# Kernel tuning notes

Measured on AMD Instinct MI355X. Metric: run time of the kernel, lower is better.

Reference implementation:

```python
import jax, jax.numpy as jnp
import numpy as np
from jax import lax

HEADS = 8
HEAD_C = 16  # attention_channels // heads = 128 // 8


def setup_inputs() -> dict:
    key = jax.random.key(0)
    ks = jax.random.split(key, 16)
    N, I, H, W = 8, 128, 36, 36
    R, C, A, O = 128, 128, 128, 128  # recurrent, common, attention, out channels
    s = lambda *sh: 0.05
    inp = {
        'x': jax.random.normal(ks[0], (N, I, H, W), jnp.float32),
        # input 1x1 conv (Accumulate of single Conv, bias init 0)
        'w_in': jax.random.normal(ks[1], (R, I), jnp.float32) * 0.05,
        'b_in': jnp.zeros((R,), jnp.float32),
        # 3x3 conv on cat([x, h]) -> common channels
        'w_conv': jax.random.normal(ks[2], (C, 2 * R, 3, 3), jnp.float32) * 0.05,
        'b_conv': jnp.zeros((C,), jnp.float32),
        # q/k/v 1x1 projections (no bias)
        'wq': jax.random.normal(ks[3], (A, C), jnp.float32) * 0.05,
        'wk': jax.random.normal(ks[4], (A, C), jnp.float32) * 0.05,
        'wv': jax.random.normal(ks[5], (A, C), jnp.float32) * 0.05,
        # gate 1x1 projections on cat([z, a]) (C + A inputs)
        'w_i': jax.random.normal(ks[6], (R, C + A), jnp.float32) * 0.05,
        'b_i': jnp.full((R,), -1.0, jnp.float32),  # init_input
        'w_f': jax.random.normal(ks[7], (R, C + A), jnp.float32) * 0.05,
        'b_f': jnp.full((R,), 1.0, jnp.float32),   # init_forget
        'w_g': jax.random.normal(ks[8], (R, C + A), jnp.float32) * 0.05,
        'b_g': jnp.zeros((R,), jnp.float32),
        'w_o': jax.random.normal(ks[9], (R, C + A), jnp.float32) * 0.05,
        'b_o': jnp.zeros((R,), jnp.float32),
        # output 1x1 conv
        'w_out': jax.random.normal(ks[10], (O, R), jnp.float32) * 0.05,
        'b_out': jnp.zeros((O,), jnp.float32),
    }
    return inp


def _conv1x1(w, x, b=None):
    y = jnp.einsum('oi,nihw->nohw', w, x)
    if b is not None:
        y = y + b[None, :, None, None]
    return y


def reference(x, w_in, b_in, w_conv, b_conv, wq, wk, wv,
              w_i, b_i, w_f, b_f, w_g, b_g, w_o, b_o, w_out, b_out):
    # first timestep: past is empty -> h = c = 0
    xt = jnp.tanh(_conv1x1(w_in, x, b_in))          # [N, R, H, W]
    h0 = jnp.zeros_like(xt)
    c0 = jnp.zeros_like(xt)
    xh = jnp.concatenate([xt, h0], axis=1)          # groups=1 -> plain concat
    z = lax.conv_general_dilated(xh, w_conv, (1, 1), 'SAME') + b_conv[None, :, None, None]
    N, C, H, W = z.shape
    HW = H * W
    q = _conv1x1(wq, z).reshape(N, HEADS, HEAD_C, HW)
    k = _conv1x1(wk, z).reshape(N, HEADS, HEAD_C, HW)
    v = _conv1x1(wv, z).reshape(N, HEADS, HEAD_C, HW)
    # spatial attention over H*W tokens per head
    w_attn = jax.nn.softmax(jnp.einsum('nhcq,nhcd->nhqd', q, k), axis=-1)  # [N,heads,HW,HW]
    a = jnp.einsum('nhcd,nhqd->nhcq', v, w_attn).reshape(N, -1, H, W)      # [N,A,H,W]
    za = jnp.concatenate([z, a], axis=1)
    i = jax.nn.sigmoid(_conv1x1(w_i, za, b_i))
    f = jax.nn.sigmoid(_conv1x1(w_f, za, b_f))
    g = jnp.tanh(_conv1x1(w_g, za, b_g))
    o = jax.nn.sigmoid(_conv1x1(w_o, za, b_o))
    c = f * c0 + i * g
    h = o * jnp.tanh(c)  # dropout p=0 -> identity
    return _conv1x1(w_out, h, b_out)
```

## Files before the change

### kernel.cpp

```cpp
#include <hip/hip_runtime.h>
#include <hip/hip_bf16.h>
#include <math.h>

typedef __hip_bfloat16 bf16;
typedef __attribute__((ext_vector_type(8))) short frag8;
typedef __attribute__((ext_vector_type(4))) float f32x4;
typedef __attribute__((ext_vector_type(16))) float f32x16;
typedef __attribute__((ext_vector_type(2))) unsigned int u32x2;
typedef __attribute__((ext_vector_type(4))) unsigned int u32x4;

#define HW  1296
#define CH  128
#define TT  1327104

__device__ __forceinline__ float b2f(bf16 v) { return __bfloat162float(v); }
__device__ __forceinline__ float bits2f(unsigned short u) {
    return __uint_as_float(((unsigned)u) << 16);
}
__device__ __forceinline__ float frcp(float x) { return __builtin_amdgcn_rcpf(x); }
__device__ __forceinline__ float fsigm(float x) { return frcp(1.0f + __expf(-x)); }
__device__ __forceinline__ float ftanh(float x) {
    float xc = fminf(15.0f, fmaxf(-15.0f, x));
    float e = __expf(2.0f * xc);
    return (e - 1.0f) * frcp(e + 1.0f);
}
__device__ __forceinline__ int packrh(float a, float b) {
    unsigned ua = __float_as_uint(a) + 0x8000u;
    unsigned ub = __float_as_uint(b) + 0x8000u;
    return (int)__builtin_amdgcn_perm(ub, ua, 0x07060302);
}
__device__ __forceinline__ int2 pack4(float a, float b, float c, float d) {
    int2 r; r.x = packrh(a, b); r.y = packrh(c, d); return r;
}
__device__ __forceinline__ unsigned cvtpk(float a, float b) {
    unsigned r;
    asm("v_cvt_pk_bf16_f32 %0, %1, %2" : "=v"(r) : "v"(a), "v"(b));
    return r;
}

__device__ __forceinline__ int detect_f32(const void* w) {
    const short4* p = (const short4*)w;
    short4 v = p[threadIdx.x & 63];
    int bad = 0;
    #pragma unroll
    for (int j = 0; j < 4; ++j) {
        float f = bits2f(((const unsigned short*)&v)[j]);
        if (!(fabsf(f) <= 100.0f)) bad = 1;
    }
    return __any(bad) ? 1 : 0;
}

__global__ __launch_bounds__(256) void k_prep(
    const void* w_in, const void* w_conv, const void* wq, const void* wk, const void* wv,
    const void* w_i, const void* w_g, const void* w_o, const void* w_out,
    const void* b_in, const void* b_conv, const void* b_i, const void* b_g,
    const void* b_o, const void* b_out,
    bf16* __restrict__ Wdst, float* __restrict__ Bdst, bf16* __restrict__ Pad)
{
    int idx = blockIdx.x * 256 + threadIdx.x;
    const int f = detect_f32(w_in);
    if (idx < 327680) {
        const void* src; int si;
        if (idx < 16384)       { src = w_in; si = idx; }
        else if (idx < 163840) { int j = idx - 16384; int tap = j >> 14, rem = j & 16383;
                                 int o = rem >> 7, r = rem & 127;
                                 src = w_conv; si = o * 2304 + r * 9 + tap; }
        else if (idx < 212992) { int j = idx - 163840; int o = j >> 7, i = j & 127;
                                 int ws_ = o >> 7;
                                 src = ws_ == 0 ? wq : ws_ == 1 ? wk : wv;
                                 si = (o & 127) * 128 + i; }
        else if (idx < 311296) { int j = idx - 212992; int g = j >> 15, rem = j & 32767;
                                 int o = rem >> 8, k = rem & 255;
                                 src = g == 0 ? w_i : g == 1 ? w_g : w_o; si = o * 256 + k; }
        else                   { int j = idx - 311296; int o = j >> 7, i = j & 127;
                                 src = w_out; si = o * 128 + i; }
        float v = f ? ((const float*)src)[si] : b2f(((const bf16*)src)[si]);
        if (idx >= 163840 && idx < 180224) v *= 1.4426950408889634f;
        Wdst[idx] = __float2bfloat16(v);
    } else if (idx < 328448) {
        int j = idx - 327680; int b = j >> 7, e = j & 127;
        const void* src = b == 0 ? b_in : b == 1 ? b_conv : b == 2 ? b_i
                        : b == 3 ? b_g : b == 4 ? b_o : b_out;
        Bdst[j] = f ? ((const float*)src)[e] : b2f(((const bf16*)src)[e]);
    } else if (idx < 332544) {
        int j = idx - 328448;
        Pad[j] = __float2bfloat16(j < 2048 ? 0.0f : 1.0f);
    }
}

__global__ __launch_bounds__(256) void k_inm(const void* __restrict__ x,
                                             const void* __restrict__ wraw,
                                             const bf16* __restrict__ Wm,
                                             const float* __restrict__ bias,
                                             bf16* __restrict__ XT) {
    __shared__ short Xl[32][132];
    const int tid = threadIdx.x, wave = tid >> 6, lane = tid & 63;
    const int quad = lane >> 4, l16 = lane & 15;
    const int n = blockIdx.x;
    const int pbase = blockIdx.y * 32;
    const int obase = blockIdx.z * 32 + (wave & 1) * 16;
    const int pstrip = (wave >> 1) * 16;
    const int f = detect_f32(wraw);

    frag8 WF[4];
    #pragma unroll
    for (int kc = 0; kc < 4; ++kc)
        WF[kc] = *(const frag8*)&Wm[(obase + l16) * CH + kc * 32 + quad * 8];

    #pragma unroll
    for (int rep = 0; rep < 4; ++rep) {
        int u = tid + rep * 256;
        int i = u >> 3;
        int p4 = (u & 7) * 4;
        int p = pbase + p4;
        int pc = p < HW ? p : HW - 4;
        size_t gi = (size_t)n * CH * HW + (size_t)i * HW + pc;
        short4 s;
        if (f) {
            float4 fv = *(const float4*)((const float*)x + gi);
            int2 pk = pack4(fv.x, fv.y, fv.z, fv.w);
            s = *(short4*)&pk;
        } else {
            s = *(const short4*)((const bf16*)x + gi);
        }
        Xl[p4 + 0][i] = s.x; Xl[p4 + 1][i] = s.y;
        Xl[p4 + 2][i] = s.z; Xl[p4 + 3][i] = s.w;
    }
    __syncthreads();

    const int pl = pstrip + l16;
    f32x4 acc = {0.f, 0.f, 0.f, 0.f};
    #pragma unroll
    for (int kc = 0; kc < 4; ++kc) {
        int k = kc * 32 + quad * 8;
        short4 b0 = *(const short4*)&Xl[pl][k];
        short4 b1 = *(const short4*)&Xl[pl][k + 4];
        frag8 bf = {b0.x, b0.y, b0.z, b0.w, b1.x, b1.y, b1.z, b1.w};
        acc = __builtin_amdgcn_mfma_f32_16x16x32_bf16(WF[kc], bf, acc, 0, 0, 0);
    }

    int p = pbase + pstrip + l16;
    if (p < HW) {
        int og = obase + quad * 4;
        int2 pk = pack4(ftanh(acc[0] + bias[og + 0]), ftanh(acc[1] + bias[og + 1]),
                        ftanh(acc[2] + bias[og + 2]), ftanh(acc[3] + bias[og + 3]));
        *(int2*)((short*)XT + ((size_t)n * HW + p) * CH + og) = pk;
    }
}

__global__ __launch_bounds__(512) void k_cq(
    const bf16* __restrict__ XT, const bf16* __restrict__ Wc,
    const float* __restrict__ bc, const bf16* __restrict__ Wqkv,
    const bf16* __restrict__ Pad,
    bf16* __restrict__ Zb, bf16* __restrict__ Qb, bf16* __restrict__ Kb,
    bf16* __restrict__ Vb)
{
    __shared__ short Zl[32][136];
    __shared__ float Rd[4][4][4][64];
    const int tid = threadIdx.x, w = tid >> 6, lane = tid & 63;
    const int quad = lane >> 4, l16 = lane & 15;
    const int n = blockIdx.x;
    const int pbase = blockIdx.y * 32;
    const bf16* actn = XT + (size_t)n * HW * CH;

    const int o4 = w & 3, tg = w >> 2;
    const int obase = o4 * 32;
    const int p1 = pbase + l16, p2 = pbase + 16 + l16;
    const bool p1ok = p1 < HW, p2ok = p2 < HW;
    const int h1 = p1 / 36, w1 = p1 - h1 * 36;
    const int h2 = p2 / 36, w2 = p2 - h2 * 36;
    const bf16* zrow = Pad + quad * 8;

    f32x4 acc[2][2];
    #pragma unroll
    for (int of = 0; of < 2; ++of) {
        acc[of][0] = (f32x4){0.f, 0.f, 0.f, 0.f};
        acc[of][1] = (f32x4){0.f, 0.f, 0.f, 0.f};
    }

    const int tap0 = tg ? 5 : 0, tap1 = tg ? 9 : 5;
    for (int tap = tap0; tap < tap1; ++tap) {
        const int dy = tap / 3 - 1, dx = tap - (tap / 3) * 3 - 1;
        const bool ok1 = p1ok && (unsigned)(h1 + dy) < 36u && (unsigned)(w1 + dx) < 36u;
        const bool ok2 = p2ok && (unsigned)(h2 + dy) < 36u && (unsigned)(w2 + dx) < 36u;
        const int sh = dy * 36 + dx;
        const bf16* a1 = ok1 ? actn + (size_t)(p1 + sh) * CH + quad * 8 : zrow;
        const bf16* a2 = ok2 ? actn + (size_t)(p2 + sh) * CH + quad * 8 : zrow;
        const bf16* wp0 = Wc + tap * 16384 + (obase + l16) * CH + quad * 8;
        const bf16* wp1 = Wc + tap * 16384 + (obase + 16 + l16) * CH + quad * 8;
        frag8 A1[4], A2[4], W0[4], W1[4];
        #pragma unroll
        for (int kc = 0; kc < 4; ++kc) {
            A1[kc] = *(const frag8*)&a1[kc * 32];
            A2[kc] = *(const frag8*)&a2[kc * 32];
            W0[kc] = *(const frag8*)&wp0[kc * 32];
            W1[kc] = *(const frag8*)&wp1[kc * 32];
        }
        #pragma unroll
        for (int kc = 0; kc < 4; ++kc) {
            acc[0][0] = __builtin_amdgcn_mfma_f32_16x16x32_bf16(W0[kc], A1[kc], acc[0][0], 0, 0, 0);
            acc[0][1] = __builtin_amdgcn_mfma_f32_16x16x32_bf16(W0[kc], A2[kc], acc[0][1], 0, 0, 0);
            acc[1][0] = __builtin_amdgcn_mfma_f32_16x16x32_bf16(W1[kc], A1[kc], acc[1][0], 0, 0, 0);
            acc[1][1] = __builtin_amdgcn_mfma_f32_16x16x32_bf16(W1[kc], A2[kc], acc[1][1], 0, 0, 0);
        }
    }

    if (tg == 1) {
        #pragma unroll
        for (int of = 0; of < 2; ++of)
            #pragma unroll
            for (int pt = 0; pt < 2; ++pt)
                #pragma unroll
                for (int r = 0; r < 4; ++r)
                    Rd[o4][of * 2 + pt][r][lane] = acc[of][pt][r];
    }
    __syncthreads();
    if (tg == 0) {
        #pragma unroll
        for (int of = 0; of < 2; ++of) {
            #pragma unroll
            for (int pt = 0; pt < 2; ++pt) {
                #pragma unroll
                for (int r = 0; r < 4; ++r)
                    acc[of][pt][r] += Rd[o4][of * 2 + pt][r][lane];
                int og = obase + of * 16 + quad * 4;
                int pl = pt * 16 + l16;
                int p = pbase + pl;
                int2 pk = pack4(acc[of][pt][0] + bc[og + 0], acc[of][pt][1] + bc[og + 1],
                                acc[of][pt][2] + bc[og + 2], acc[of][pt][3] + bc[og + 3]);
                *(int2*)&Zl[pl][og] = pk;
                if (p < HW)
                    *(int2*)((short*)Zb + ((size_t)n * HW + p) * CH + og) = pk;
            }
        }
    }
    __syncthreads();

    for (int ot = w; ot < 12; ot += 8) {
        const bool vt = (ot >= 8);
        const int ob = ot * 32;
        frag8 B1[4], B2[4], W0a[4], W1a[4];
        #pragma unroll
        for (int kc = 0; kc < 4; ++kc) {
            int ko = kc * 32 + quad * 8;
            B1[kc]  = *(const frag8*)&Zl[l16][ko];
            B2[kc]  = *(const frag8*)&Zl[16 + l16][ko];
            W0a[kc] = *(const frag8*)&Wqkv[(size_t)(ob + l16) * CH + ko];
            W1a[kc] = *(const frag8*)&Wqkv[(size_t)(ob + 16 + l16) * CH + ko];
        }

        f32x4 qacc[2][2];
        #pragma unroll
        for (int of = 0; of < 2; ++of) {
            qacc[of][0] = (f32x4){0.f, 0.f, 0.f, 0.f};
            qacc[of][1] = (f32x4){0.f, 0.f, 0.f, 0.f};
        }
        #pragma unroll
        for (int kc = 0; kc < 4; ++kc) {
            if (vt) {
                qacc[0][0] = __builtin_amdgcn_mfma_f32_16x16x32_bf16(B1[kc], W0a[kc], qacc[0][0], 0, 0, 0);
                qacc[0][1] = __builtin_amdgcn_mfma_f32_16x16x32_bf16(B2[kc], W0a[kc], qacc[0][1], 0, 0, 0);
                qacc[1][0] = __builtin_amdgcn_mfma_f32_16x16x32_bf16(B1[kc], W1a[kc], qacc[1][0], 0, 0, 0);
                qacc[1][1] = __builtin_amdgcn_mfma_f32_16x16x32_bf16(B2[kc], W1a[kc], qacc[1][1], 0, 0, 0);
            } else {
                qacc[0][0] = __builtin_amdgcn_mfma_f32_16x16x32_bf16(W0a[kc], B1[kc], qacc[0][0], 0, 0, 0);
                qacc[0][1] = __builtin_amdgcn_mfma_f32_16x16x32_bf16(W0a[kc], B2[kc], qacc[0][1], 0, 0, 0);
                qacc[1][0] = __builtin_amdgcn_mfma_f32_16x16x32_bf16(W1a[kc], B1[kc], qacc[1][0], 0, 0, 0);
                qacc[1][1] = __builtin_amdgcn_mfma_f32_16x16x32_bf16(W1a[kc], B2[kc], qacc[1][1], 0, 0, 0);
            }
        }

        if (vt) {
            #pragma unroll
            for (int of = 0; of < 2; ++of) {
                int ov = ob + of * 16 - 256 + l16;
                #pragma unroll
                for (int pt = 0; pt < 2; ++pt) {
                    int p4 = pbase + pt * 16 + quad * 4;
                    if (p4 >= HW) continue;
                    int2 pk = pack4(qacc[of][pt][0], qacc[of][pt][1], qacc[of][pt][2], qacc[of][pt][3]);
                    *(int2*)((short*)Vb + ((size_t)n * CH + ov) * HW + p4) = pk;
                }
            }
        } else {
            #pragma unroll
            for (int of = 0; of < 2; ++of) {
                int ogq = ob + of * 16 + quad * 4;
                int which = ogq >> 7, ol = ogq & 127;
                bf16* dst = which == 0 ? Qb : Kb;
                #pragma unroll
                for (int pt = 0; pt < 2; ++pt) {
                    int p = pbase + pt * 16 + l16;
                    if (p >= HW) continue;
                    size_t di = (((size_t)n * 8 + (ol >> 4)) * HW + p) * 16 + (ol & 15);
                    int2 pk = pack4(qacc[of][pt][0], qacc[of][pt][1], qacc[of][pt][2], qacc[of][pt][3]);
                    *(int2*)((short*)dst + di) = pk;
                }
            }
        }
    }
}

__global__ __launch_bounds__(256) void k_cell(
    const bf16* __restrict__ Zb, const bf16* __restrict__ Ab,
    const bf16* __restrict__ Wg, const float* __restrict__ bg,
    const bf16* __restrict__ Wo, const float* __restrict__ bo,
    void* __restrict__ out, const void* __restrict__ wraw)
{
    __shared__ short Hl[16][136];
    const int tid = threadIdx.x, w = tid >> 6, lane = tid & 63;
    const int quad = lane >> 4, l16 = lane & 15;
    const int n = blockIdx.x;
    const int pbase = blockIdx.y * 16;
    const int f32f = detect_f32(wraw);
    const bf16* zn = Zb + (size_t)n * HW * CH;
    const bf16* an = Ab + (size_t)n * HW * CH;

    const int obase = w * 32;
    const int p1 = pbase + l16;

    f32x4 acc[3][2];
    #pragma unroll
    for (int g = 0; g < 3; ++g) {
        acc[g][0] = (f32x4){0.f, 0.f, 0.f, 0.f};
        acc[g][1] = (f32x4){0.f, 0.f, 0.f, 0.f};
    }

    frag8 GB[2];
    frag8 GW[2][6];

    #define LOADG(KC, BUF)                                                           \
    {                                                                                \
        const bf16* src = ((KC) >= 4) ? an : zn;                                     \
        const int ko = ((KC) & 3) * 32 + quad * 8;                                   \
        GB[BUF] = *(const frag8*)&src[(size_t)p1 * CH + ko];                         \
        _Pragma("unroll")                                                            \
        for (int g = 0; g < 3; ++g) {                                                \
            _Pragma("unroll")                                                        \
            for (int of = 0; of < 2; ++of)                                           \
                GW[BUF][g * 2 + of] = *(const frag8*)&Wg[g * 32768 +                 \
                    (obase + of * 16 + l16) * 256 + (KC) * 32 + quad * 8];           \
        }                                                                            \
    }

    LOADG(0, 0);
    #pragma unroll
    for (int kc = 0; kc < 8; ++kc) {
        const int cur = kc & 1;
        if (kc < 7) LOADG(kc + 1, cur ^ 1);
        #pragma unroll
        for (int g = 0; g < 3; ++g) {
            #pragma unroll
            for (int of = 0; of < 2; ++of)
                acc[g][of] = __builtin_amdgcn_mfma_f32_16x16x32_bf16(
                    GW[cur][g * 2 + of], GB[cur], acc[g][of], 0, 0, 0);
        }
    }
    #undef LOADG

    #pragma unroll
    for (int of = 0; of < 2; ++of) {
        int og = obase + of * 16 + quad * 4;
        float hv[4];
        #pragma unroll
        for (int r = 0; r < 4; ++r) {
            int o = og + r;
            float iv = fsigm(acc[0][of][r] + bg[o]);
            float gv = ftanh(acc[1][of][r] + bg[128 + o]);
            float ov = fsigm(acc[2][of][r] + bg[256 + o]);
            hv[r] = ov * ftanh(iv * gv);
        }
        *(int2*)&Hl[l16][og] = pack4(hv[0], hv[1], hv[2], hv[3]);
    }

    frag8 OW[2][4];
    #pragma unroll
    for (int of = 0; of < 2; ++of)
        #pragma unroll
        for (int kc = 0; kc < 4; ++kc)
            OW[of][kc] = *(const frag8*)&Wo[(size_t)(obase + of * 16 + l16) * CH
                                            + kc * 32 + quad * 8];
    __syncthreads();

    f32x4 oc[2];
    oc[0] = (f32x4){0.f, 0.f, 0.f, 0.f};
    oc[1] = (f32x4){0.f, 0.f, 0.f, 0.f};
    #pragma unroll
    for (int kc = 0; kc < 4; ++kc) {
        int k = kc * 32 + quad * 8;
        short4 h0 = *(const short4*)&Hl[l16][k];
        short4 h1 = *(const short4*)&Hl[l16][k + 4];
        frag8 af = {h0.x, h0.y, h0.z, h0.w, h1.x, h1.y, h1.z, h1.w};
        #pragma unroll
        for (int of = 0; of < 2; ++of)
            oc[of] = __builtin_amdgcn_mfma_f32_16x16x32_bf16(af, OW[of][kc], oc[of], 0, 0, 0);
    }
    int p4 = pbase + quad * 4;
    #pragma unroll
    for (int of = 0; of < 2; ++of) {
        int o = obase + of * 16 + l16;
        float bv = bo[o];
        size_t di = ((size_t)n * CH + o) * HW + p4;
        if (f32f) {
            float4 fv = {oc[of][0] + bv, oc[of][1] + bv, oc[of][2] + bv, oc[of][3] + bv};
            *(float4*)&((float*)out)[di] = fv;
        } else {
            int2 pk = pack4(oc[of][0] + bv, oc[of][1] + bv, oc[of][2] + bv, oc[of][3] + bv);
            *(int2*)&((short*)out)[di] = pk;
        }
    }
}

__global__ __launch_bounds__(512) void k_attn(const bf16* __restrict__ Qg,
                                              const bf16* __restrict__ Kg,
                                              const bf16* __restrict__ Vcf,
                                              const bf16* __restrict__ Pad,
                                              bf16* __restrict__ A) {
    __shared__ float Lc[4][9][64];

    const int tid = threadIdx.x;
    const int w = tid >> 6, lane = tid & 63;
    const int l32 = lane & 31, hi = lane >> 5;
    const int qw = w & 3, dq = w >> 2;
    const int n = blockIdx.x;
    const int head = blockIdx.z;
    const int qb = blockIdx.y * 128 + qw * 32;
    const int qtok = qb + l32;

    const short* Qh = (const short*)Qg + ((size_t)(n * 8 + head)) * HW * 16;
    const short* Kh = (const short*)Kg + ((size_t)(n * 8 + head)) * HW * 16;
    const short* Vh = (const short*)Vcf + ((size_t)n * CH + head * 16) * HW;

    frag8 qf = *(const frag8*)&Qh[(size_t)(qtok < HW ? qtok : 0) * 16 + hi * 8];

    const short* Vrow = (l32 < 16) ? Vh + (size_t)l32 * HW
                      : (const short*)(Pad + (l32 == 16 ? 2048 : 0));

    const f32x16 zero16 = {};
    f32x16 Oacc = {};

    auto KLD = [&](int dd) -> frag8 {
        return *(const frag8*)&Kh[(size_t)(dd + l32) * 16 + hi * 8];
    };
    auto VLD = [&](int dd) -> frag8 {
        return *(const frag8*)&Vrow[dd + hi * 8];
    };

    const int c0 = dq ? 20 : 0;
    frag8 kf  = KLD(c0 * 32);
    frag8 kf2 = KLD(c0 * 32 + 32);
    frag8 va  = VLD(c0 * 32);
    frag8 vb  = VLD(c0 * 32 + 16);
    f32x16 S = __builtin_amdgcn_mfma_f32_32x32x16_bf16(kf, qf, zero16, 0, 0, 0);

    for (int it = 0; it < 20; ++it) {
        const int d0 = (c0 + it) * 32;
        frag8 kn  = KLD(d0 + 64);
        frag8 van = VLD(d0 + 32);
        frag8 vbn = VLD(d0 + 48);
        f32x16 Sn = __builtin_amdgcn_mfma_f32_32x32x16_bf16(kf2, qf, zero16, 0, 0, 0);

        float p[16];
        #pragma unroll
        for (int r = 0; r < 16; ++r) p[r] = __builtin_amdgcn_exp2f(S[r]);

        #pragma unroll
        for (int hh = 0; hh < 2; ++hh) {
            unsigned P0 = cvtpk(p[hh * 8 + 0], p[hh * 8 + 1]);
            unsigned P1 = cvtpk(p[hh * 8 + 2], p[hh * 8 + 3]);
            unsigned P2 = cvtpk(p[hh * 8 + 4], p[hh * 8 + 5]);
            unsigned P3 = cvtpk(p[hh * 8 + 6], p[hh * 8 + 7]);
            u32x2 s02 = __builtin_amdgcn_permlane32_swap(P0, P2, false, false);
            u32x2 s13 = __builtin_amdgcn_permlane32_swap(P1, P3, false, false);
            u32x4 bw = {s02[0], s13[0], s02[1], s13[1]};
            frag8 pf = __builtin_bit_cast(frag8, bw);
            Oacc = __builtin_amdgcn_mfma_f32_32x32x16_bf16(hh ? vb : va, pf, Oacc, 0, 0, 0);
        }
        kf2 = kn; va = van; vb = vbn; S = Sn;
    }

    if (dq) {
        float p[8];
        #pragma unroll
        for (int r = 0; r < 8; ++r) p[r] = __builtin_amdgcn_exp2f(S[r]);
        unsigned P0 = cvtpk(p[0], p[1]);
        unsigned P1 = cvtpk(p[2], p[3]);
        unsigned P2 = cvtpk(p[4], p[5]);
        unsigned P3 = cvtpk(p[6], p[7]);
        u32x2 s02 = __builtin_amdgcn_permlane32_swap(P0, P2, false, false);
        u32x2 s13 = __builtin_amdgcn_permlane32_swap(P1, P3, false, false);
        u32x4 bw = {s02[0], s13[0], s02[1], s13[1]};
        frag8 pf = __builtin_bit_cast(frag8, bw);
        Oacc = __builtin_amdgcn_mfma_f32_32x32x16_bf16(va, pf, Oacc, 0, 0, 0);
        #pragma unroll
        for (int r = 0; r < 8; ++r) Lc[qw][r][lane] = Oacc[r];
        Lc[qw][8][lane] = Oacc[8];
    }
    __syncthreads();
    if (dq == 0) {
        #pragma unroll
        for (int r = 0; r < 8; ++r) Oacc[r] += Lc[qw][r][lane];
        float lsum = Oacc[8] + Lc[qw][8][lane];
        u32x2 lb = __builtin_amdgcn_permlane32_swap(__float_as_uint(lsum),
                                                    __float_as_uint(lsum), false, false);
        float inv = frcp(__uint_as_float(lb[0]));
        if (qtok < HW) {
            short* An = (short*)A + ((size_t)n * HW + qtok) * CH + head * 16;
            int2 pk0 = pack4(Oacc[0] * inv, Oacc[1] * inv, Oacc[2] * inv, Oacc[3] * inv);
            int2 pk1 = pack4(Oacc[4] * inv, Oacc[5] * inv, Oacc[6] * inv, Oacc[7] * inv);
            *(int2*)&An[hi * 4] = pk0;
            *(int2*)&An[8 + hi * 4] = pk1;
        }
    }
}

extern "C" void kernel_launch(void* const* d_in, const int* in_sizes, int n_in,
                              void* d_out, int out_size, void* d_ws, size_t ws_size,
                              hipStream_t stream) {
    char* ws = (char*)d_ws;
    bf16*  Wst  = (bf16*)(ws + 256);
    float* Bst  = (float*)(ws + 655616);
    bf16*  Pad  = (bf16*)(ws + 786432);
    bf16*  XT   = (bf16*)(ws + 1048576);
    bf16*  Zb   = XT + TT;
    bf16*  Qb   = Zb + TT;
    bf16*  Kb   = Qb + TT;
    bf16*  Vb   = Kb + TT;
    bf16*  Ab   = Vb + TT;

    k_prep<<<1300, 256, 0, stream>>>(d_in[1], d_in[3], d_in[5], d_in[6], d_in[7],
                                     d_in[8], d_in[12], d_in[14], d_in[16],
                                     d_in[2], d_in[4], d_in[9], d_in[13], d_in[15], d_in[17],
                                     Wst, Bst, Pad);
    k_inm<<<dim3(8, 41, 4), 256, 0, stream>>>(d_in[0], d_in[1], Wst, Bst, XT);
    k_cq<<<dim3(8, 41), 512, 0, stream>>>(XT, Wst + 16384, Bst + 128, Wst + 163840,
                                          Pad, Zb, Qb, Kb, Vb);
    k_attn<<<dim3(8, 11, 8), 512, 0, stream>>>(Qb, Kb, Vb, Pad, Ab);
    k_cell<<<dim3(8, 81), 256, 0, stream>>>(Zb, Ab, Wst + 212992, Bst + 256,
                                            Wst + 311296, Bst + 640, d_out, d_in[1]);
}
```

Before: 186.4 us.

## Stage conv input halo in LDS and split 3x3 conv by output channels

The 3x3 conv inside the fused conv+QKV kernel now loads a 112-row halo of the tanh input into shared memory once per block. The 9 taps then read their shifted rows from LDS instead of issuing repeated global loads. Work is split across the 8 waves by 16-channel output slices rather than by tap groups, which removes the cross-wave reduction through shared memory and one barrier. This adds about 34 KB of LDS per block, which may reduce occupancy, and each wave now runs all 9 taps serially.

Result: faster. 170.0 us (median of 2 runs) (-8.8%).

```diff
diff --git a/kernel.cpp b/kernel.cpp
--- a/kernel.cpp
+++ b/kernel.cpp
@@ -155,84 +155,72 @@
     bf16* __restrict__ Zb, bf16* __restrict__ Qb, bf16* __restrict__ Kb,
     bf16* __restrict__ Vb)
 {
+    __shared__ short Xs[128][136];
     __shared__ short Zl[32][136];
-    __shared__ float Rd[4][4][4][64];
     const int tid = threadIdx.x, w = tid >> 6, lane = tid & 63;
     const int quad = lane >> 4, l16 = lane & 15;
     const int n = blockIdx.x;
     const int pbase = blockIdx.y * 32;
-    const bf16* actn = XT + (size_t)n * HW * CH;
-
-    const int o4 = w & 3, tg = w >> 2;
-    const int obase = o4 * 32;
-    const int p1 = pbase + l16, p2 = pbase + 16 + l16;
-    const bool p1ok = p1 < HW, p2ok = p2 < HW;
+    const bf16* XTn = XT + (size_t)n * HW * CH;
+
+    {
+        frag8 st[4];
+        int rowv[4], chv[4];
+        #pragma unroll
+        for (int i = 0; i < 4; ++i) {
+            int ci = i * 512 + tid;
+            int row = ci >> 4, ch = ci & 15;
+            rowv[i] = row; chv[i] = ch;
+            int p = pbase - 37 + row;
+            const bf16* src = (row < 112 && (unsigned)p < (unsigned)HW)
+                            ? &XTn[(size_t)p * CH + ch * 8] : &Pad[ch * 8];
+            st[i] = *(const frag8*)src;
+        }
+        #pragma unroll
+        for (int i = 0; i < 4; ++i)
+            *(frag8*)&Xs[rowv[i]][chv[i] * 8] = st[i];
+    }
+    __syncthreads();
+
+    const int obase = w * 16;
+    const int p1 = pbase + l16, p2 = p1 + 16;
     const int h1 = p1 / 36, w1 = p1 - h1 * 36;
     const int h2 = p2 / 36, w2 = p2 - h2 * 36;
-    const bf16* zrow = Pad + quad * 8;
-
-    f32x4 acc[2][2];
-    #pragma unroll
-    for (int of = 0; of < 2; ++of) {
-        acc[of][0] = (f32x4){0.f, 0.f, 0.f, 0.f};
-        acc[of][1] = (f32x4){0.f, 0.f, 0.f, 0.f};
-    }
-
-    const int tap0 = tg ? 5 : 0, tap1 = tg ? 9 : 5;
-    for (int tap = tap0; tap < tap1; ++tap) {
+    const bool p1ok = p1 < HW, p2ok = p2 < HW;
+
+    f32x4 acc[2];
+    acc[0] = (f32x4){0.f, 0.f, 0.f, 0.f};
+    acc[1] = (f32x4){0.f, 0.f, 0.f, 0.f};
+
+    #pragma unroll
+    for (int tap = 0; tap < 9; ++tap) {
         const int dy = tap / 3 - 1, dx = tap - (tap / 3) * 3 - 1;
         const bool ok1 = p1ok && (unsigned)(h1 + dy) < 36u && (unsigned)(w1 + dx) < 36u;
         const bool ok2 = p2ok && (unsigned)(h2 + dy) < 36u && (unsigned)(w2 + dx) < 36u;
         const int sh = dy * 36 + dx;
-        const bf16* a1 = ok1 ? actn + (size_t)(p1 + sh) * CH + quad * 8 : zrow;
-        const bf16* a2 = ok2 ? actn + (size_t)(p2 + sh) * CH + quad * 8 : zrow;
-        const bf16* wp0 = Wc + tap * 16384 + (obase + l16) * CH + quad * 8;
-        const bf16* wp1 = Wc + tap * 16384 + (obase + 16 + l16) * CH + quad * 8;
-        frag8 A1[4], A2[4], W0[4], W1[4];
+        const int r1 = ok1 ? 37 + l16 + sh : 112;
+        const int r2 = ok2 ? 53 + l16 + sh : 112;
+        const bf16* wp = Wc + tap * 16384 + (obase + l16) * CH + quad * 8;
         #pragma unroll
         for (int kc = 0; kc < 4; ++kc) {
-            A1[kc] = *(const frag8*)&a1[kc * 32];
-            A2[kc] = *(const frag8*)&a2[kc * 32];
-            W0[kc] = *(const frag8*)&wp0[kc * 32];
-            W1[kc] = *(const frag8*)&wp1[kc * 32];
-        }
-        #pragma unroll
-        for (int kc = 0; kc < 4; ++kc) {
-            acc[0][0] = __builtin_amdgcn_mfma_f32_16x16x32_bf16(W0[kc], A1[kc], acc[0][0], 0, 0, 0);
-            acc[0][1] = __builtin_amdgcn_mfma_f32_16x16x32_bf16(W0[kc], A2[kc], acc[0][1], 0, 0, 0);
-            acc[1][0] = __builtin_amdgcn_mfma_f32_16x16x32_bf16(W1[kc], A1[kc], acc[1][0], 0, 0, 0);
-            acc[1][1] = __builtin_amdgcn_mfma_f32_16x16x32_bf16(W1[kc], A2[kc], acc[1][1], 0, 0, 0);
-        }
-    }
-
-    if (tg == 1) {
-        #pragma unroll
-        for (int of = 0; of < 2; ++of)
-            #pragma unroll
-            for (int pt = 0; pt < 2; ++pt)
-                #pragma unroll
-                for (int r = 0; r < 4; ++r)
-                    Rd[o4][of * 2 + pt][r][lane] = acc[of][pt][r];
-    }
-    __syncthreads();
-    if (tg == 0) {
-        #pragma unroll
-        for (int of = 0; of < 2; ++of) {
-            #pragma unroll
-            for (int pt = 0; pt < 2; ++pt) {
-                #pragma unroll
-                for (int r = 0; r < 4; ++r)
-                    acc[of][pt][r] += Rd[o4][of * 2 + pt][r][lane];
-                int og = obase + of * 16 + quad * 4;
-                int pl = pt * 16 + l16;
-                int p = pbase + pl;
-                int2 pk = pack4(acc[of][pt][0] + bc[og + 0], acc[of][pt][1] + bc[og + 1],
-                                acc[of][pt][2] + bc[og + 2], acc[of][pt][3] + bc[og + 3]);
-                *(int2*)&Zl[pl][og] = pk;
-                if (p < HW)
-                    *(int2*)((short*)Zb + ((size_t)n * HW + p) * CH + og) = pk;
-            }
-        }
+            frag8 a1 = *(const frag8*)&Xs[r1][kc * 32 + quad * 8];
+            frag8 a2 = *(const frag8*)&Xs[r2][kc * 32 + quad * 8];
+            frag8 wf = *(const frag8*)&wp[kc * 32];
+            acc[0] = __builtin_amdgcn_mfma_f32_16x16x32_bf16(wf, a1, acc[0], 0, 0, 0);
+            acc[1] = __builtin_amdgcn_mfma_f32_16x16x32_bf16(wf, a2, acc[1], 0, 0, 0);
+        }
+    }
+
+    const int og = obase + quad * 4;
+    #pragma unroll
+    for (int pt = 0; pt < 2; ++pt) {
+        int pl = pt * 16 + l16;
+        int p = pbase + pl;
+        int2 pk = pack4(acc[pt][0] + bc[og + 0], acc[pt][1] + bc[og + 1],
+                        acc[pt][2] + bc[og + 2], acc[pt][3] + bc[og + 3]);
+        *(int2*)&Zl[pl][og] = pk;
+        if (p < HW)
+            *(int2*)((short*)Zb + ((size_t)n * HW + p) * CH + og) = pk;
     }
     __syncthreads();
 
```
